# Kernel tuning notes

Measured on AMD Instinct MI355X. Metric: run time of the kernel, lower is better.

## Reference

```python
import jax, jax.numpy as jnp
import numpy as np

N_Q_HEADS = 16
N_KV_HEADS = 4
HEAD_DIM = 64
GROUPS = N_Q_HEADS // N_KV_HEADS


def apply_rope(xq, xk, cos, sin):
    # xq: [B,S,Hq,D], xk: [B,S,Hkv,D]; cos/sin: [S, D/2]
    def rot(t):
        tr = t[..., 0::2]
        ti = t[..., 1::2]
        c = cos[None, :, None, :]
        s = sin[None, :, None, :]
        out_r = tr * c - ti * s
        out_i = tr * s + ti * c
        # interleave back: [..., D/2, 2] -> [..., D]
        return jnp.stack([out_r, out_i], axis=-1).reshape(t.shape)
    return rot(xq), rot(xk)


def setup_inputs() -> dict:
    key = jax.random.key(0)
    ks = jax.random.split(key, 8)
    B, S, DIM = 2, 2048, 1024
    x = jax.random.normal(ks[0], (B, S, DIM), jnp.float32)
    # RoPE frequencies (llama-style): theta_i = 10000^(-2i/D), angles = pos * theta
    inv_freq = 1.0 / (10000.0 ** (jnp.arange(0, HEAD_DIM, 2, dtype=jnp.float32) / HEAD_DIM))
    angles = jnp.arange(S, dtype=jnp.float32)[:, None] * inv_freq[None, :]  # [S, D/2]
    freqs_cos = jnp.cos(angles)
    freqs_sin = jnp.sin(angles)
    # additive causal mask [1,1,S,S]
    neg = jnp.float32(-1e9)
    mask = jnp.where(jnp.tril(jnp.ones((S, S), bool)), 0.0, neg)[None, None]
    scale = 0.02
    wq = jax.random.normal(ks[1], (DIM, N_Q_HEADS * HEAD_DIM), jnp.float32) * scale
    wk = jax.random.normal(ks[2], (DIM, N_KV_HEADS * HEAD_DIM), jnp.float32) * scale
    wv = jax.random.normal(ks[3], (DIM, N_KV_HEADS * HEAD_DIM), jnp.float32) * scale
    wo = jax.random.normal(ks[4], (DIM, DIM), jnp.float32) * scale
    return {"x": x, "start_pos": 0, "freqs_cos": freqs_cos, "freqs_sin": freqs_sin,
            "mask": mask, "wq": wq, "wk": wk, "wv": wv, "wo": wo}


def reference(x, start_pos, freqs_cos, freqs_sin, mask, wq, wk, wv, wo):
    B, S, DIM = x.shape
    xq = (x @ wq).reshape(B, S, N_Q_HEADS, HEAD_DIM)
    xk = (x @ wk).reshape(B, S, N_KV_HEADS, HEAD_DIM)
    xv = (x @ wv).reshape(B, S, N_KV_HEADS, HEAD_DIM)
    xq, xk = apply_rope(xq, xk, freqs_cos, freqs_sin)
    # seq_len > 1: prefill path, no KV-cache read. repeat_kv: expand kv heads by GROUPS.
    keys = jnp.repeat(xk, GROUPS, axis=2)    # [B,S,Hq,D]
    values = jnp.repeat(xv, GROUPS, axis=2)
    q = xq.transpose(0, 2, 1, 3)             # [B,H,S,D]
    k = keys.transpose(0, 2, 1, 3)
    v = values.transpose(0, 2, 1, 3)
    scores = jnp.einsum('bhqd,bhkd->bhqk', q, k) / jnp.sqrt(jnp.float32(HEAD_DIM))
    scores = scores + mask
    probs = jax.nn.softmax(scores, axis=-1)
    attn = jnp.einsum('bhqk,bhkd->bhqd', probs, v)  # [B,H,S,D]
    attn = attn.transpose(0, 2, 1, 3).reshape(B, S, DIM)
    return attn @ wo
```

## Files before the change

kernel.cpp:

```cpp
#include <hip/hip_runtime.h>

typedef __bf16 bf16_t;
typedef __bf16 bf16x8 __attribute__((ext_vector_type(8)));
typedef __bf16 bf16x4 __attribute__((ext_vector_type(4)));
typedef float f32x4 __attribute__((ext_vector_type(4)));
typedef short short4v __attribute__((ext_vector_type(4)));

#if __has_builtin(__builtin_amdgcn_exp2f)
#define EXP2F __builtin_amdgcn_exp2f
#else
#define EXP2F exp2f
#endif

#define BATCH 2
#define SEQ   2048
#define DIM   1024
#define NQH   16
#define NKVH  4
#define HD    64
#define ROWS  (BATCH*SEQ)
#define QKVN  1536
#define QSCALE 0.1803368801111f

static __device__ __forceinline__ short4v as_s4(bf16x4 v) {
    union { bf16x4 b; short4v s; } u; u.b = v; return u.s;
}

static __device__ __forceinline__ void gld16(const bf16_t* g, bf16_t* l) {
    __builtin_amdgcn_global_load_lds((const __attribute__((address_space(1))) void*)g,
                                     (__attribute__((address_space(3))) void*)l,
                                     16, 0, 0);
}

__global__ __launch_bounds__(256) void cast_x_kernel(const float* __restrict__ x,
                                                     bf16_t* __restrict__ o) {
    size_t i = ((size_t)blockIdx.x * 256 + threadIdx.x) * 4;
    float4 v = *(const float4*)(x + i);
    bf16x4 r;
    r[0] = (bf16_t)v.x; r[1] = (bf16_t)v.y; r[2] = (bf16_t)v.z; r[3] = (bf16_t)v.w;
    *(bf16x4*)(o + i) = r;
}

__global__ __launch_bounds__(256) void transpose_w_all(const float* __restrict__ wq,
                                                       const float* __restrict__ wk,
                                                       const float* __restrict__ wv,
                                                       const float* __restrict__ wo,
                                                       bf16_t* __restrict__ WqkvT,
                                                       bf16_t* __restrict__ WoT) {
    int bid = blockIdx.x;
    const float* src; bf16_t* dst; int N, nt, kt2;
    if (bid < 256)      { src = wq; dst = WqkvT;                      N = 1024; int i = bid;       nt = i & 15; kt2 = i >> 4; }
    else if (bid < 320) { src = wk; dst = WqkvT + (size_t)1024*1024;  N = 256;  int i = bid - 256; nt = i & 3;  kt2 = i >> 2; }
    else if (bid < 384) { src = wv; dst = WqkvT + (size_t)1280*1024;  N = 256;  int i = bid - 320; nt = i & 3;  kt2 = i >> 2; }
    else                { src = wo; dst = WoT;                        N = 1024; int i = bid - 384; nt = i & 15; kt2 = i >> 4; }

    __shared__ float tile[64][65];
    int t = threadIdx.x;
    {
        int r = t >> 2, cb = (t & 3) * 16;
        const float* s = src + (size_t)(kt2 * 64 + r) * N + nt * 64 + cb;
#pragma unroll
        for (int j = 0; j < 16; j += 4) {
            float4 v = *(const float4*)(s + j);
            tile[r][cb + j + 0] = v.x; tile[r][cb + j + 1] = v.y;
            tile[r][cb + j + 2] = v.z; tile[r][cb + j + 3] = v.w;
        }
    }
    __syncthreads();
    {
        int n = t >> 2, kb = (t & 3) * 16;
        union { bf16_t h[16]; uint4 u[2]; } pk;
#pragma unroll
        for (int j = 0; j < 16; ++j) pk.h[j] = (bf16_t)tile[kb + j][n];
        bf16_t* d = dst + (size_t)(nt * 64 + n) * 1024 + kt2 * 64 + kb;
        ((uint4*)d)[0] = pk.u[0];
        ((uint4*)d)[1] = pk.u[1];
    }
}

__global__ __launch_bounds__(256, 2) void gemm_qkv_kernel(const bf16_t* __restrict__ A,
                                                          const bf16_t* __restrict__ Bt,
                                                          const float* __restrict__ fcos,
                                                          const float* __restrict__ fsin,
                                                          bf16_t* __restrict__ Qb,
                                                          bf16_t* __restrict__ Kb,
                                                          bf16_t* __restrict__ Vt) {
    const int K = 1024;
    __shared__ __align__(16) bf16_t As[128 * 32];
    __shared__ __align__(16) bf16_t Bs[128 * 32];
    int t = threadIdx.x;
    int w = t >> 6, L = t & 63, quad = L >> 4, l15 = L & 15;
    int wr = (w >> 1) * 64, wc = (w & 1) * 64;
    int bnb = blockIdx.x;
    int bn = bnb * 128, bm = blockIdx.y * 128;

    const bf16_t* Ag0 = A  + (size_t)(bm + w * 32 + (L >> 2)) * K + (L & 3) * 8;
    const bf16_t* Ag1 = Ag0 + (size_t)16 * K;
    const bf16_t* Bg0 = Bt + (size_t)(bn + w * 32 + (L >> 2)) * K + (L & 3) * 8;
    const bf16_t* Bg1 = Bg0 + (size_t)16 * K;
    bf16_t* Al = As + w * 1024;
    bf16_t* Bl = Bs + w * 1024;

    f32x4 acc[4][4] = {};

    for (int k0 = 0; k0 < K; k0 += 32) {
        __syncthreads();
        gld16(Ag0 + k0, Al);
        gld16(Ag1 + k0, Al + 512);
        gld16(Bg0 + k0, Bl);
        gld16(Bg1 + k0, Bl + 512);
        __syncthreads();

        bf16x8 a[4], b[4];
#pragma unroll
        for (int i = 0; i < 4; ++i) {
            a[i] = ((const bf16x8*)As)[(wr + 16 * i + l15) * 4 + quad];
            b[i] = ((const bf16x8*)Bs)[(wc + 16 * i + l15) * 4 + quad];
        }
#pragma unroll
        for (int i = 0; i < 4; ++i)
#pragma unroll
            for (int j = 0; j < 4; ++j)
                acc[i][j] = __builtin_amdgcn_mfma_f32_16x16x32_bf16(a[i], b[j], acc[i][j], 0, 0, 0);
    }

    int region = (bnb >= 10) ? 2 : (bnb >= 8) ? 1 : 0;
#pragma unroll
    for (int i = 0; i < 4; ++i) {
        int row0 = bm + wr + 16 * i + quad * 4;
        int b = row0 >> 11, s0 = row0 & 2047;
#pragma unroll
        for (int j = 0; j < 4; ++j) {
            int col = bn + wc + 16 * j + l15;
            if (region == 2) {
                int kvh = (col >> 6) - 20, d = col & 63;
                bf16x4 o;
#pragma unroll
                for (int r = 0; r < 4; ++r) o[r] = (bf16_t)acc[i][j][r];
                *(bf16x4*)(Vt + ((size_t)((b * NKVH + kvh) * HD + d)) * SEQ + s0) = o;
            } else {
                int d = col & 63, fi = d >> 1;
                int odd = col & 1;
#pragma unroll
                for (int r = 0; r < 4; ++r) {
                    int s = s0 + r;
                    float v = acc[i][j][r];
                    float p = __shfl_xor(v, 1);
                    float c = fcos[s * 32 + fi], sn = fsin[s * 32 + fi];
                    float o = odd ? (p * sn + v * c) : (v * c - p * sn);
                    if (region == 0) {
                        int h = col >> 6;
                        Qb[((size_t)((b * NQH + h) * SEQ + s)) * HD + d] = (bf16_t)(o * QSCALE);
                    } else {
                        int kvh = (col >> 6) - 16;
                        Kb[((size_t)((b * NKVH + kvh) * SEQ + s)) * HD + d] = (bf16_t)o;
                    }
                }
            }
        }
    }
}

__global__ __launch_bounds__(256, 2) void gemm_bt_kernel(const bf16_t* __restrict__ A,
                                                         const bf16_t* __restrict__ Bt,
                                                         float* __restrict__ C,
                                                         int M, int N, int K) {
    __shared__ __align__(16) bf16_t As[128 * 32];
    __shared__ __align__(16) bf16_t Bs[128 * 32];
    int t = threadIdx.x;
    int w = t >> 6, L = t & 63, quad = L >> 4, l15 = L & 15;
    int wr = (w >> 1) * 64, wc = (w & 1) * 64;
    int bn = blockIdx.x * 128, bm = blockIdx.y * 128;

    const bf16_t* Ag0 = A  + (size_t)(bm + w * 32 + (L >> 2)) * K + (L & 3) * 8;
    const bf16_t* Ag1 = Ag0 + (size_t)16 * K;
    const bf16_t* Bg0 = Bt + (size_t)(bn + w * 32 + (L >> 2)) * K + (L & 3) * 8;
    const bf16_t* Bg1 = Bg0 + (size_t)16 * K;
    bf16_t* Al = As + w * 1024;
    bf16_t* Bl = Bs + w * 1024;

    f32x4 acc[4][4] = {};

    for (int k0 = 0; k0 < K; k0 += 32) {
        __syncthreads();
        gld16(Ag0 + k0, Al);
        gld16(Ag1 + k0, Al + 512);
        gld16(Bg0 + k0, Bl);
        gld16(Bg1 + k0, Bl + 512);
        __syncthreads();

        bf16x8 a[4], b[4];
#pragma unroll
        for (int i = 0; i < 4; ++i) {
            a[i] = ((const bf16x8*)As)[(wr + 16 * i + l15) * 4 + quad];
            b[i] = ((const bf16x8*)Bs)[(wc + 16 * i + l15) * 4 + quad];
        }
#pragma unroll
        for (int i = 0; i < 4; ++i)
#pragma unroll
            for (int j = 0; j < 4; ++j)
                acc[i][j] = __builtin_amdgcn_mfma_f32_16x16x32_bf16(a[i], b[j], acc[i][j], 0, 0, 0);
    }

#pragma unroll
    for (int i = 0; i < 4; ++i) {
        int row = bm + wr + 16 * i + quad * 4;
#pragma unroll
        for (int j = 0; j < 4; ++j) {
            int col = bn + wc + 16 * j + l15;
            float* cp = C + (size_t)row * N + col;
#pragma unroll
            for (int r = 0; r < 4; ++r)
                cp[(size_t)r * N] = acc[i][j][r];
        }
    }
}

__global__ __launch_bounds__(512, 2) void attn_kernel(const bf16_t* __restrict__ Qb,
                                                      const bf16_t* __restrict__ Kb,
                                                      const bf16_t* __restrict__ Vt,
                                                      bf16_t* __restrict__ Ob) {
    int bq = blockIdx.x, h = blockIdx.y, b = blockIdx.z;
    int kv = h >> 2;
    int t = threadIdx.x, w = t >> 6, lane = t & 63, quad = lane >> 4, l15 = lane & 15;

    __shared__ __align__(16) bf16_t Ks[64 * 64];
    __shared__ __align__(16) bf16_t Vs[64 * 64];

    const bf16_t* Qbase = Qb + ((size_t)(b * NQH + h)) * SEQ * HD;
    const bf16_t* Kbase = Kb + ((size_t)(b * NKVH + kv)) * SEQ * HD;
    const bf16_t* Vbase = Vt + ((size_t)(b * NKVH + kv)) * HD * SEQ;

    int sm = t >> 3, spos = t & 7, skc = spos ^ (sm & 7);
    const bf16_t* ksrc = Kbase + (size_t)sm * HD + skc * 8;
    const bf16_t* vsrc = Vbase + (size_t)sm * SEQ + skc * 8;

#pragma unroll 1
    for (int ph = 0; ph < 2; ++ph) {
        int qt = ph ? (15 - bq) : bq;
        int Q0 = qt * 128;
        int wq = Q0 + 16 * w + l15;
        int myktmax = (Q0 + 16 * w + 15) >> 6;
        int ktmax = (Q0 + 127) >> 6;

        bf16x8 aq[2];
#pragma unroll
        for (int ks = 0; ks < 2; ++ks)
            aq[ks] = *(const bf16x8*)(Qbase + (size_t)wq * HD + ks * 32 + quad * 8);

        f32x4 acc_o[4] = {};
        float rs = 0.f;

        uint4 kpre = *(const uint4*)ksrc;
        uint4 vpre = *(const uint4*)vsrc;

        for (int kt = 0; kt <= ktmax; ++kt) {
            __syncthreads();
            ((uint4*)Ks)[t] = kpre;
            ((uint4*)Vs)[t] = vpre;
            __syncthreads();
            if (kt < ktmax) {
                kpre = *(const uint4*)(ksrc + (size_t)(kt + 1) * 64 * HD);
                vpre = *(const uint4*)(vsrc + (size_t)(kt + 1) * 64);
            }
            if (kt > myktmax) continue;

            f32x4 st[4];
#pragma unroll
            for (int x = 0; x < 4; ++x) {
                int key = 16 * x + l15;
                bf16x8 ak0 = ((const bf16x8*)Ks)[key * 8 + ((0 + quad) ^ (key & 7))];
                bf16x8 ak1 = ((const bf16x8*)Ks)[key * 8 + ((4 + quad) ^ (key & 7))];
                f32x4 z = {0.f, 0.f, 0.f, 0.f};
                z = __builtin_amdgcn_mfma_f32_16x16x32_bf16(ak0, aq[0], z, 0, 0, 0);
                z = __builtin_amdgcn_mfma_f32_16x16x32_bf16(ak1, aq[1], z, 0, 0, 0);
                st[x] = z;
            }

            short4v bp[4];
            if (kt == myktmax) {
                int kb = kt * 64 + quad * 4;
#pragma unroll
                for (int x = 0; x < 4; ++x) {
                    bf16x4 pb;
#pragma unroll
                    for (int r = 0; r < 4; ++r) {
                        float p = (kb + 16 * x + r <= wq) ? EXP2F(st[x][r]) : 0.f;
                        rs += p; pb[r] = (bf16_t)p;
                    }
                    bp[x] = as_s4(pb);
                }
            } else {
#pragma unroll
                for (int x = 0; x < 4; ++x) {
                    bf16x4 pb;
#pragma unroll
                    for (int r = 0; r < 4; ++r) {
                        float p = EXP2F(st[x][r]);
                        rs += p; pb[r] = (bf16_t)p;
                    }
                    bp[x] = as_s4(pb);
                }
            }

#pragma unroll
            for (int dt = 0; dt < 4; ++dt) {
                int d = 16 * dt + l15;
#pragma unroll
                for (int x = 0; x < 4; ++x) {
                    int pos = (2 * x + (quad >> 1)) ^ (d & 7);
                    bf16x4 av = *(const bf16x4*)(Vs + d * 64 + pos * 8 + (quad & 1) * 4);
                    acc_o[dt] = __builtin_amdgcn_mfma_f32_16x16x16bf16_1k(as_s4(av), bp[x], acc_o[dt], 0, 0, 0);
                }
            }
        }

        rs += __shfl_xor(rs, 16);
        rs += __shfl_xor(rs, 32);
        float rinv = 1.0f / rs;
        bf16_t* obase = Ob + (size_t)(b * SEQ + wq) * DIM + h * HD;
#pragma unroll
        for (int dt = 0; dt < 4; ++dt) {
            bf16x4 o;
#pragma unroll
            for (int r = 0; r < 4; ++r) o[r] = (bf16_t)(acc_o[dt][r] * rinv);
            *(bf16x4*)(obase + 16 * dt + quad * 4) = o;
        }
    }
}

extern "C" void kernel_launch(void* const* d_in, const int* in_sizes, int n_in,
                              void* d_out, int out_size, void* d_ws, size_t ws_size,
                              hipStream_t stream) {
    const float* x    = (const float*)d_in[0];
    const float* fcos = (const float*)d_in[2];
    const float* fsin = (const float*)d_in[3];
    const float* wq   = (const float*)d_in[5];
    const float* wk   = (const float*)d_in[6];
    const float* wv   = (const float*)d_in[7];
    const float* wo   = (const float*)d_in[8];
    float* out = (float*)d_out;

    char* ws = (char*)d_ws;
    bf16_t* Xb    = (bf16_t*)(ws + 0);
    bf16_t* Attnb = Xb;
    bf16_t* WqkvT = (bf16_t*)(ws + 8388608);
    bf16_t* WoT   = (bf16_t*)(ws + 11534336);
    bf16_t* Qb    = (bf16_t*)(ws + 13631488);
    bf16_t* Kb    = (bf16_t*)(ws + 22020096);
    bf16_t* Vt    = (bf16_t*)(ws + 24117248);

    cast_x_kernel<<<ROWS * DIM / 1024, 256, 0, stream>>>(x, Xb);
    transpose_w_all<<<640, 256, 0, stream>>>(wq, wk, wv, wo, WqkvT, WoT);

    gemm_qkv_kernel<<<dim3(QKVN / 128, ROWS / 128), 256, 0, stream>>>(Xb, WqkvT, fcos, fsin, Qb, Kb, Vt);

    attn_kernel<<<dim3(8, NQH, BATCH), 512, 0, stream>>>(Qb, Kb, Vt, Attnb);

    gemm_bt_kernel<<<dim3(DIM / 128, ROWS / 128), 256, 0, stream>>>(Attnb, WoT, out, ROWS, DIM, DIM);
}
```

Measured before the change: 186.8 us.

## Deepen GEMM K tiles with swizzled LDS, remap block ids, split attention tiles

Both GEMMs now stage 64-wide K slices in LDS with an XOR-swizzled layout, which halves the number of barrier pairs per K loop and aims to reduce LDS bank conflicts. Block indices are remapped to a 1D grid with an XCD-aware swizzle to improve L2 locality. The attention kernel no longer has each block process a pair of q tiles (bq and 15-bq) in two phases. Each block now handles one q tile, launches twice as many blocks, raises the occupancy hint to 4, and fuses the score MFMA with exp. The cost is more LDS per GEMM block, and attention work is balanced only by the launch order instead of by pairing tiles.

New measurement: 194.9 us. 4.4% more time.

```diff
diff --git a/kernel.cpp b/kernel.cpp
--- a/kernel.cpp
+++ b/kernel.cpp
@@ -86,42 +86,53 @@
                                                           bf16_t* __restrict__ Kb,
                                                           bf16_t* __restrict__ Vt) {
     const int K = 1024;
-    __shared__ __align__(16) bf16_t As[128 * 32];
-    __shared__ __align__(16) bf16_t Bs[128 * 32];
+    __shared__ __align__(16) bf16_t As[128 * 64];
+    __shared__ __align__(16) bf16_t Bs[128 * 64];
     int t = threadIdx.x;
     int w = t >> 6, L = t & 63, quad = L >> 4, l15 = L & 15;
     int wr = (w >> 1) * 64, wc = (w & 1) * 64;
-    int bnb = blockIdx.x;
-    int bn = bnb * 128, bm = blockIdx.y * 128;
-
-    const bf16_t* Ag0 = A  + (size_t)(bm + w * 32 + (L >> 2)) * K + (L & 3) * 8;
-    const bf16_t* Ag1 = Ag0 + (size_t)16 * K;
-    const bf16_t* Bg0 = Bt + (size_t)(bn + w * 32 + (L >> 2)) * K + (L & 3) * 8;
-    const bf16_t* Bg1 = Bg0 + (size_t)16 * K;
-    bf16_t* Al = As + w * 1024;
-    bf16_t* Bl = Bs + w * 1024;
+
+    int xid = blockIdx.x;
+    int sw = (xid & 7) * 48 + (xid >> 3);
+    int bnb = sw % 12;
+    int bm = (sw / 12) * 128, bn = bnb * 128;
+
+    int srow = L >> 3;
+    int schunk = (L & 7) ^ srow;
+    const bf16_t* Ag = A  + (size_t)(bm + w * 32 + srow) * K + schunk * 8;
+    const bf16_t* Bg = Bt + (size_t)(bn + w * 32 + srow) * K + schunk * 8;
+    bf16_t* Al = As + w * 2048;
+    bf16_t* Bl = Bs + w * 2048;
+
+    int rs0 = quad ^ (l15 & 7);
+    int rs1 = (4 + quad) ^ (l15 & 7);
 
     f32x4 acc[4][4] = {};
 
-    for (int k0 = 0; k0 < K; k0 += 32) {
-        __syncthreads();
-        gld16(Ag0 + k0, Al);
-        gld16(Ag1 + k0, Al + 512);
-        gld16(Bg0 + k0, Bl);
-        gld16(Bg1 + k0, Bl + 512);
-        __syncthreads();
-
-        bf16x8 a[4], b[4];
-#pragma unroll
-        for (int i = 0; i < 4; ++i) {
-            a[i] = ((const bf16x8*)As)[(wr + 16 * i + l15) * 4 + quad];
-            b[i] = ((const bf16x8*)Bs)[(wc + 16 * i + l15) * 4 + quad];
-        }
-#pragma unroll
-        for (int i = 0; i < 4; ++i)
-#pragma unroll
-            for (int j = 0; j < 4; ++j)
-                acc[i][j] = __builtin_amdgcn_mfma_f32_16x16x32_bf16(a[i], b[j], acc[i][j], 0, 0, 0);
+    for (int k0 = 0; k0 < K; k0 += 64) {
+        __syncthreads();
+#pragma unroll
+        for (int c = 0; c < 4; ++c) {
+            gld16(Ag + (size_t)(c * 8) * K + k0, Al + c * 512);
+            gld16(Bg + (size_t)(c * 8) * K + k0, Bl + c * 512);
+        }
+        __syncthreads();
+
+#pragma unroll
+        for (int kk = 0; kk < 2; ++kk) {
+            int rsl = kk ? rs1 : rs0;
+            bf16x8 a[4], b[4];
+#pragma unroll
+            for (int i = 0; i < 4; ++i) {
+                a[i] = ((const bf16x8*)As)[(wr + 16 * i + l15) * 8 + rsl];
+                b[i] = ((const bf16x8*)Bs)[(wc + 16 * i + l15) * 8 + rsl];
+            }
+#pragma unroll
+            for (int i = 0; i < 4; ++i)
+#pragma unroll
+                for (int j = 0; j < 4; ++j)
+                    acc[i][j] = __builtin_amdgcn_mfma_f32_16x16x32_bf16(a[i], b[j], acc[i][j], 0, 0, 0);
+        }
     }
 
     int region = (bnb >= 10) ? 2 : (bnb >= 8) ? 1 : 0;
@@ -163,43 +174,54 @@
 
 __global__ __launch_bounds__(256, 2) void gemm_bt_kernel(const bf16_t* __restrict__ A,
                                                          const bf16_t* __restrict__ Bt,
-                                                         float* __restrict__ C,
-                                                         int M, int N, int K) {
-    __shared__ __align__(16) bf16_t As[128 * 32];
-    __shared__ __align__(16) bf16_t Bs[128 * 32];
+                                                         float* __restrict__ C) {
+    const int K = 1024, N = 1024;
+    __shared__ __align__(16) bf16_t As[128 * 64];
+    __shared__ __align__(16) bf16_t Bs[128 * 64];
     int t = threadIdx.x;
     int w = t >> 6, L = t & 63, quad = L >> 4, l15 = L & 15;
     int wr = (w >> 1) * 64, wc = (w & 1) * 64;
-    int bn = blockIdx.x * 128, bm = blockIdx.y * 128;
-
-    const bf16_t* Ag0 = A  + (size_t)(bm + w * 32 + (L >> 2)) * K + (L & 3) * 8;
-    const bf16_t* Ag1 = Ag0 + (size_t)16 * K;
-    const bf16_t* Bg0 = Bt + (size_t)(bn + w * 32 + (L >> 2)) * K + (L & 3) * 8;
-    const bf16_t* Bg1 = Bg0 + (size_t)16 * K;
-    bf16_t* Al = As + w * 1024;
-    bf16_t* Bl = Bs + w * 1024;
+
+    int xid = blockIdx.x;
+    int sw = (xid & 7) * 32 + (xid >> 3);
+    int bm = (sw >> 3) * 128, bn = (sw & 7) * 128;
+
+    int srow = L >> 3;
+    int schunk = (L & 7) ^ srow;
+    const bf16_t* Ag = A  + (size_t)(bm + w * 32 + srow) * K + schunk * 8;
+    const bf16_t* Bg = Bt + (size_t)(bn + w * 32 + srow) * K + schunk * 8;
+    bf16_t* Al = As + w * 2048;
+    bf16_t* Bl = Bs + w * 2048;
+
+    int rs0 = quad ^ (l15 & 7);
+    int rs1 = (4 + quad) ^ (l15 & 7);
 
     f32x4 acc[4][4] = {};
 
-    for (int k0 = 0; k0 < K; k0 += 32) {
-        __syncthreads();
-        gld16(Ag0 + k0, Al);
-        gld16(Ag1 + k0, Al + 512);
-        gld16(Bg0 + k0, Bl);
-        gld16(Bg1 + k0, Bl + 512);
-        __syncthreads();
-
-        bf16x8 a[4], b[4];
-#pragma unroll
-        for (int i = 0; i < 4; ++i) {
-            a[i] = ((const bf16x8*)As)[(wr + 16 * i + l15) * 4 + quad];
-            b[i] = ((const bf16x8*)Bs)[(wc + 16 * i + l15) * 4 + quad];
-        }
-#pragma unroll
-        for (int i = 0; i < 4; ++i)
-#pragma unroll
-            for (int j = 0; j < 4; ++j)
-                acc[i][j] = __builtin_amdgcn_mfma_f32_16x16x32_bf16(a[i], b[j], acc[i][j], 0, 0, 0);
+    for (int k0 = 0; k0 < K; k0 += 64) {
+        __syncthreads();
+#pragma unroll
+        for (int c = 0; c < 4; ++c) {
+            gld16(Ag + (size_t)(c * 8) * K + k0, Al + c * 512);
+            gld16(Bg + (size_t)(c * 8) * K + k0, Bl + c * 512);
+        }
+        __syncthreads();
+
+#pragma unroll
+        for (int kk = 0; kk < 2; ++kk) {
+            int rsl = kk ? rs1 : rs0;
+            bf16x8 a[4], b[4];
+#pragma unroll
+            for (int i = 0; i < 4; ++i) {
+                a[i] = ((const bf16x8*)As)[(wr + 16 * i + l15) * 8 + rsl];
+                b[i] = ((const bf16x8*)Bs)[(wc + 16 * i + l15) * 8 + rsl];
+            }
+#pragma unroll
+            for (int i = 0; i < 4; ++i)
+#pragma unroll
+                for (int j = 0; j < 4; ++j)
+                    acc[i][j] = __builtin_amdgcn_mfma_f32_16x16x32_bf16(a[i], b[j], acc[i][j], 0, 0, 0);
+        }
     }
 
 #pragma unroll
@@ -216,12 +238,18 @@
     }
 }
 
-__global__ __launch_bounds__(512, 2) void attn_kernel(const bf16_t* __restrict__ Qb,
+__global__ __launch_bounds__(512, 4) void attn_kernel(const bf16_t* __restrict__ Qb,
                                                       const bf16_t* __restrict__ Kb,
                                                       const bf16_t* __restrict__ Vt,
                                                       bf16_t* __restrict__ Ob) {
-    int bq = blockIdx.x, h = blockIdx.y, b = blockIdx.z;
-    int kv = h >> 2;
+    int id = blockIdx.x;
+    int sw = (id & 7) * 64 + (id >> 3);
+    int b  = sw >> 8;
+    int kv = (sw >> 6) & 3;
+    int h  = kv * 4 + ((sw >> 4) & 3);
+    int bq = sw & 15;
+    int qt = 15 - bq;
+
     int t = threadIdx.x, w = t >> 6, lane = t & 63, quad = lane >> 4, l15 = lane & 15;
 
     __shared__ __align__(16) bf16_t Ks[64 * 64];
@@ -235,37 +263,36 @@
     const bf16_t* ksrc = Kbase + (size_t)sm * HD + skc * 8;
     const bf16_t* vsrc = Vbase + (size_t)sm * SEQ + skc * 8;
 
-#pragma unroll 1
-    for (int ph = 0; ph < 2; ++ph) {
-        int qt = ph ? (15 - bq) : bq;
-        int Q0 = qt * 128;
-        int wq = Q0 + 16 * w + l15;
-        int myktmax = (Q0 + 16 * w + 15) >> 6;
-        int ktmax = (Q0 + 127) >> 6;
-
-        bf16x8 aq[2];
-#pragma unroll
-        for (int ks = 0; ks < 2; ++ks)
-            aq[ks] = *(const bf16x8*)(Qbase + (size_t)wq * HD + ks * 32 + quad * 8);
-
-        f32x4 acc_o[4] = {};
-        float rs = 0.f;
-
-        uint4 kpre = *(const uint4*)ksrc;
-        uint4 vpre = *(const uint4*)vsrc;
-
-        for (int kt = 0; kt <= ktmax; ++kt) {
-            __syncthreads();
-            ((uint4*)Ks)[t] = kpre;
-            ((uint4*)Vs)[t] = vpre;
-            __syncthreads();
-            if (kt < ktmax) {
-                kpre = *(const uint4*)(ksrc + (size_t)(kt + 1) * 64 * HD);
-                vpre = *(const uint4*)(vsrc + (size_t)(kt + 1) * 64);
-            }
-            if (kt > myktmax) continue;
-
-            f32x4 st[4];
+    int Q0 = qt * 128;
+    int wq = Q0 + 16 * w + l15;
+    int myktmax = (Q0 + 16 * w + 15) >> 6;
+    int ktmax = (Q0 + 127) >> 6;
+
+    bf16x8 aq[2];
+#pragma unroll
+    for (int ks = 0; ks < 2; ++ks)
+        aq[ks] = *(const bf16x8*)(Qbase + (size_t)wq * HD + ks * 32 + quad * 8);
+
+    f32x4 acc_o[4] = {};
+    float rs = 0.f;
+
+    uint4 kpre = *(const uint4*)ksrc;
+    uint4 vpre = *(const uint4*)vsrc;
+
+    for (int kt = 0; kt <= ktmax; ++kt) {
+        __syncthreads();
+        ((uint4*)Ks)[t] = kpre;
+        ((uint4*)Vs)[t] = vpre;
+        __syncthreads();
+        if (kt < ktmax) {
+            kpre = *(const uint4*)(ksrc + (size_t)(kt + 1) * 64 * HD);
+            vpre = *(const uint4*)(vsrc + (size_t)(kt + 1) * 64);
+        }
+        if (kt > myktmax) continue;
+
+        short4v bp[4];
+        if (kt == myktmax) {
+            int kb = kt * 64 + quad * 4;
 #pragma unroll
             for (int x = 0; x < 4; ++x) {
                 int key = 16 * x + l15;
@@ -274,58 +301,55 @@
                 f32x4 z = {0.f, 0.f, 0.f, 0.f};
                 z = __builtin_amdgcn_mfma_f32_16x16x32_bf16(ak0, aq[0], z, 0, 0, 0);
                 z = __builtin_amdgcn_mfma_f32_16x16x32_bf16(ak1, aq[1], z, 0, 0, 0);
-                st[x] = z;
-            }
-
-            short4v bp[4];
-            if (kt == myktmax) {
-                int kb = kt * 64 + quad * 4;
-#pragma unroll
-                for (int x = 0; x < 4; ++x) {
-                    bf16x4 pb;
-#pragma unroll
-                    for (int r = 0; r < 4; ++r) {
-                        float p = (kb + 16 * x + r <= wq) ? EXP2F(st[x][r]) : 0.f;
-                        rs += p; pb[r] = (bf16_t)p;
-                    }
-                    bp[x] = as_s4(pb);
+                bf16x4 pb;
+#pragma unroll
+                for (int r = 0; r < 4; ++r) {
+                    float p = (kb + 16 * x + r <= wq) ? EXP2F(z[r]) : 0.f;
+                    rs += p; pb[r] = (bf16_t)p;
                 }
-            } else {
-#pragma unroll
-                for (int x = 0; x < 4; ++x) {
-                    bf16x4 pb;
-#pragma unroll
-                    for (int r = 0; r < 4; ++r) {
-                        float p = EXP2F(st[x][r]);
-                        rs += p; pb[r] = (bf16_t)p;
-                    }
-                    bp[x] = as_s4(pb);
+                bp[x] = as_s4(pb);
+            }
+        } else {
+#pragma unroll
+            for (int x = 0; x < 4; ++x) {
+                int key = 16 * x + l15;
+                bf16x8 ak0 = ((const bf16x8*)Ks)[key * 8 + ((0 + quad) ^ (key & 7))];
+                bf16x8 ak1 = ((const bf16x8*)Ks)[key * 8 + ((4 + quad) ^ (key & 7))];
+                f32x4 z = {0.f, 0.f, 0.f, 0.f};
+                z = __builtin_amdgcn_mfma_f32_16x16x32_bf16(ak0, aq[0], z, 0, 0, 0);
+                z = __builtin_amdgcn_mfma_f32_16x16x32_bf16(ak1, aq[1], z, 0, 0, 0);
+                bf16x4 pb;
+#pragma unroll
+                for (int r = 0; r < 4; ++r) {
+                    float p = EXP2F(z[r]);
+                    rs += p; pb[r] = (bf16_t)p;
                 }
-            }
-
-#pragma unroll
-            for (int dt = 0; dt < 4; ++dt) {
-                int d = 16 * dt + l15;
-#pragma unroll
-                for (int x = 0; x < 4; ++x) {
-                    int pos = (2 * x + (quad >> 1)) ^ (d & 7);
-                    bf16x4 av = *(const bf16x4*)(Vs + d * 64 + pos * 8 + (quad & 1) * 4);
-                    acc_o[dt] = __builtin_amdgcn_mfma_f32_16x16x16bf16_1k(as_s4(av), bp[x], acc_o[dt], 0, 0, 0);
-                }
-            }
-        }
-
-        rs += __shfl_xor(rs, 16);
-        rs += __shfl_xor(rs, 32);
-        float rinv = 1.0f / rs;
-        bf16_t* obase = Ob + (size_t)(b * SEQ + wq) * DIM + h * HD;
+                bp[x] = as_s4(pb);
+            }
+        }
+
 #pragma unroll
         for (int dt = 0; dt < 4; ++dt) {
-            bf16x4 o;
-#pragma unroll
-            for (int r = 0; r < 4; ++r) o[r] = (bf16_t)(acc_o[dt][r] * rinv);
-            *(bf16x4*)(obase + 16 * dt + quad * 4) = o;
-        }
+            int d = 16 * dt + l15;
+#pragma unroll
+            for (int x = 0; x < 4; ++x) {
+                int pos = (2 * x + (quad >> 1)) ^ (d & 7);
+                bf16x4 av = *(const bf16x4*)(Vs + d * 64 + pos * 8 + (quad & 1) * 4);
+                acc_o[dt] = __builtin_amdgcn_mfma_f32_16x16x16bf16_1k(as_s4(av), bp[x], acc_o[dt], 0, 0, 0);
+            }
+        }
+    }
+
+    rs += __shfl_xor(rs, 16);
+    rs += __shfl_xor(rs, 32);
+    float rinv = 1.0f / rs;
+    bf16_t* obase = Ob + (size_t)(b * SEQ + wq) * DIM + h * HD;
+#pragma unroll
+    for (int dt = 0; dt < 4; ++dt) {
+        bf16x4 o;
+#pragma unroll
+        for (int r = 0; r < 4; ++r) o[r] = (bf16_t)(acc_o[dt][r] * rinv);
+        *(bf16x4*)(obase + 16 * dt + quad * 4) = o;
     }
 }
 
@@ -353,9 +377,9 @@
     cast_x_kernel<<<ROWS * DIM / 1024, 256, 0, stream>>>(x, Xb);
     transpose_w_all<<<640, 256, 0, stream>>>(wq, wk, wv, wo, WqkvT, WoT);
 
-    gemm_qkv_kernel<<<dim3(QKVN / 128, ROWS / 128), 256, 0, stream>>>(Xb, WqkvT, fcos, fsin, Qb, Kb, Vt);
-
-    attn_kernel<<<dim3(8, NQH, BATCH), 512, 0, stream>>>(Qb, Kb, Vt, Attnb);
-
-    gemm_bt_kernel<<<dim3(DIM / 128, ROWS / 128), 256, 0, stream>>>(Attnb, WoT, out, ROWS, DIM, DIM);
-}
+    gemm_qkv_kernel<<<QKVN / 128 * (ROWS / 128), 256, 0, stream>>>(Xb, WqkvT, fcos, fsin, Qb, Kb, Vt);
+
+    attn_kernel<<<16 * NQH * BATCH, 512, 0, stream>>>(Qb, Kb, Vt, Attnb);
+
+    gemm_bt_kernel<<<(DIM / 128) * (ROWS / 128), 256, 0, stream>>>(Attnb, WoT, out);
+}
```
